# Kernel optimization log

Measured on AMD Instinct MI355X. Metric: run time of the kernel, lower is better.

The kernel has to match this reference:

```python
import jax, jax.numpy as jnp
import numpy as np

B, L, DM = 1, 512, 768
DS, DC, EX = 64, 4, 2
DI = EX * DM            # d_inner = 1536
DR = DM // 16           # dt_rank = 48


def setup_inputs() -> dict:
    key = jax.random.key(0)
    ks = jax.random.split(key, 12)
    s = 0.02
    inp = {
        "x": jax.random.normal(ks[0], (B, L, DM), dtype=jnp.float32),
        "ln_w": jnp.ones((DM,), jnp.float32),
        "ln_b": jnp.zeros((DM,), jnp.float32),
        "in_proj_w": jax.random.normal(ks[1], (2 * DI, DM), jnp.float32) * s,
        "conv_w": jax.random.normal(ks[2], (DI, 1, DC), jnp.float32) * s,
        "conv_b": jnp.zeros((DI,), jnp.float32),
        "x_proj_w": jax.random.normal(ks[3], (DR + 2 * DS, DI), jnp.float32) * s,
        "dt_proj_w": jax.random.normal(ks[4], (DI, DR), jnp.float32) * s,
        "dt_proj_b": jax.random.normal(ks[5], (DI,), jnp.float32) * s,
        "A_log": jnp.log(jnp.broadcast_to(jnp.arange(1, DS + 1, dtype=jnp.float32), (DI, DS))),
        "D": jnp.ones((DI,), jnp.float32),
        "out_proj_w": jax.random.normal(ks[6], (DM, DI), jnp.float32) * s,
    }
    return inp


def _layernorm(x, w, b, eps=1e-5):
    mu = jnp.mean(x, axis=-1, keepdims=True)
    var = jnp.mean((x - mu) ** 2, axis=-1, keepdims=True)
    return (x - mu) * jax.lax.rsqrt(var + eps) * w + b


def _causal_depthwise_conv(x, w, b):
    # x: [B, L, DI] -> conv over time, depthwise, causal (left pad DC-1)
    xc = jnp.transpose(x, (0, 2, 1))  # [B, DI, L]
    y = jax.lax.conv_general_dilated(
        xc, w, window_strides=(1,), padding=[(DC - 1, 0)],
        dimension_numbers=("NCH", "OIH", "NCH"), feature_group_count=DI)
    y = y + b[None, :, None]
    return jnp.transpose(y, (0, 2, 1))  # [B, L, DI]


def _selective_scan(deltaA, deltaB_u, C):
    # deltaA, deltaB_u: [B, L, DI, DS]; C: [B, L, DS]
    dA = jnp.transpose(deltaA, (1, 0, 2, 3))
    dBu = jnp.transpose(deltaB_u, (1, 0, 2, 3))
    Ct = jnp.transpose(C, (1, 0, 2))
    s0 = jnp.zeros(deltaA.shape[:1] + deltaA.shape[2:], deltaA.dtype).transpose(0, 1, 2)
    s0 = jnp.zeros((deltaA.shape[0], deltaA.shape[2], deltaA.shape[3]), deltaA.dtype)

    def step(s, inp):
        dA_t, dBu_t, C_t = inp
        s = dA_t * s + dBu_t                      # [B, DI, DS]
        y = jnp.einsum("bdn,bn->bd", s, C_t)      # [B, DI]
        return s, y

    _, ys = jax.lax.scan(step, s0, (dA, dBu, Ct))
    return jnp.transpose(ys, (1, 0, 2))           # [B, L, DI]


def reference(x, ln_w, ln_b, in_proj_w, conv_w, conv_b, x_proj_w,
              dt_proj_w, dt_proj_b, A_log, D, out_proj_w):
    residual = x
    h = _layernorm(x, ln_w, ln_b)
    xz = jnp.einsum("bld,ed->ble", h, in_proj_w)  # [B, L, 2*DI]
    x_in, z = jnp.split(xz, 2, axis=-1)
    x_in = jax.nn.silu(_causal_depthwise_conv(x_in, conv_w, conv_b))
    x_dbl = jnp.einsum("bld,ed->ble", x_in, x_proj_w)  # [B, L, DR+2*DS]
    dt, Bm, Cm = jnp.split(x_dbl, [DR, DR + DS], axis=-1)
    dt = jax.nn.softplus(jnp.einsum("blr,dr->bld", dt, dt_proj_w) + dt_proj_b)  # [B,L,DI]
    A = -jnp.exp(A_log)                                 # [DI, DS]
    deltaA = jnp.exp(dt[..., None] * A)                 # [B, L, DI, DS]
    deltaB_u = dt[..., None] * Bm[:, :, None, :] * x_in[..., None]
    y = _selective_scan(deltaA, deltaB_u, Cm)           # [B, L, DI]
    y = y + x_in * D
    y = y * jax.nn.silu(z)
    out = jnp.einsum("bld,ed->ble", y, out_proj_w)      # [B, L, DM]
    return residual + out
```

## Files before the change

kernel.cpp:

```cpp
#include <hip/hip_runtime.h>
#include <hip/hip_bf16.h>
#include <math.h>

#define L_SEQ 512
#define DM 768
#define DI 1536
#define DS 64
#define DC 4
#define DR 48
#define NBC 128
#define NP2 (NBC + DI)
#define NCF 4
#define TCF 128
#define LOG2E 1.44269504088896f

typedef __attribute__((ext_vector_type(8))) short short8;
typedef __attribute__((ext_vector_type(4))) float float4v;

#define J_LN 512
#define J_WI (2 * DI * DM / 1024)
#define J_WBC (NBC * DI / 1024)
#define J_WO (DM * DI / 1024)
#define J_WEFF ((DI / 64) * (DI / 64))
#define PREP_GRID (J_LN + J_WI + J_WBC + J_WO + J_WEFF)

__device__ __forceinline__ float bp_add(float p, int addr) {
  return p + __int_as_float(__builtin_amdgcn_ds_bpermute(addr, __float_as_int(p)));
}
__device__ __forceinline__ float lane_read(float v, int t) {
  return __int_as_float(__builtin_amdgcn_readlane(__float_as_int(v), t));
}
__device__ __forceinline__ short f2bf(float v) {
  __hip_bfloat16 h = __float2bfloat16(v);
  return *reinterpret_cast<short*>(&h);
}
__device__ __forceinline__ short8 cvt8f(const float* p, bool valid) {
  float4 u = *(const float4*)(p);
  float4 v = *(const float4*)(p + 4);
  short8 r;
  r[0] = f2bf(u.x); r[1] = f2bf(u.y); r[2] = f2bf(u.z); r[3] = f2bf(u.w);
  r[4] = f2bf(v.x); r[5] = f2bf(v.y); r[6] = f2bf(v.z); r[7] = f2bf(v.w);
  if (!valid) r = (short8)0;
  return r;
}
__device__ __forceinline__ void cvt_blk(const float* __restrict__ s,
                                        short* __restrict__ d, int b) {
  int i = b * 1024 + threadIdx.x * 4;
  float4 v = *(const float4*)(s + i);
  short4 o; o.x = f2bf(v.x); o.y = f2bf(v.y); o.z = f2bf(v.z); o.w = f2bf(v.w);
  *(short4*)(d + i) = o;
}

__device__ __forceinline__ float4v gemm32_core(
    const short* __restrict__ A, int lda, const short* __restrict__ B, int ldb,
    int K, int bx, int by, int lane, int w, float4v* red) {
  int ks = K >> 2;
  int kbeg = w * ks;
  int fr = lane & 15, koff = (lane >> 4) * 8;
  int m0 = by * 32, n0 = bx * 32;
  const short* pA0 = A + (size_t)(m0 + fr) * lda + koff + kbeg;
  const short* pA1 = pA0 + (size_t)16 * lda;
  const short* pB0 = B + (size_t)(n0 + fr) * ldb + koff + kbeg;
  const short* pB1 = pB0 + (size_t)16 * ldb;
  float4v acc00 = (float4v){0.f,0.f,0.f,0.f}, acc01 = acc00;
  float4v acc10 = acc00, acc11 = acc00;
  short8 a0A = *(const short8*)(pA0);      short8 a1A = *(const short8*)(pA1);
  short8 b0A = *(const short8*)(pB0);      short8 b1A = *(const short8*)(pB1);
  short8 a0B = *(const short8*)(pA0 + 32); short8 a1B = *(const short8*)(pA1 + 32);
  short8 b0B = *(const short8*)(pB0 + 32); short8 b1B = *(const short8*)(pB1 + 32);
  for (int k0 = 0; k0 < ks; k0 += 64) {
    short8 ca0 = a0A, ca1 = a1A, cb0 = b0A, cb1 = b1A;
    short8 da0 = a0B, da1 = a1B, db0 = b0B, db1 = b1B;
    int nA = k0 + 64; if (nA >= ks) nA = 0;
    int nB = k0 + 96; if (nB >= ks) nB = 32;
    a0A = *(const short8*)(pA0 + nA); a1A = *(const short8*)(pA1 + nA);
    b0A = *(const short8*)(pB0 + nA); b1A = *(const short8*)(pB1 + nA);
    a0B = *(const short8*)(pA0 + nB); a1B = *(const short8*)(pA1 + nB);
    b0B = *(const short8*)(pB0 + nB); b1B = *(const short8*)(pB1 + nB);
    acc00 = __builtin_amdgcn_mfma_f32_16x16x32_bf16(ca0, cb0, acc00, 0, 0, 0);
    acc01 = __builtin_amdgcn_mfma_f32_16x16x32_bf16(ca0, cb1, acc01, 0, 0, 0);
    acc10 = __builtin_amdgcn_mfma_f32_16x16x32_bf16(ca1, cb0, acc10, 0, 0, 0);
    acc11 = __builtin_amdgcn_mfma_f32_16x16x32_bf16(ca1, cb1, acc11, 0, 0, 0);
    acc00 = __builtin_amdgcn_mfma_f32_16x16x32_bf16(da0, db0, acc00, 0, 0, 0);
    acc01 = __builtin_amdgcn_mfma_f32_16x16x32_bf16(da0, db1, acc01, 0, 0, 0);
    acc10 = __builtin_amdgcn_mfma_f32_16x16x32_bf16(da1, db0, acc10, 0, 0, 0);
    acc11 = __builtin_amdgcn_mfma_f32_16x16x32_bf16(da1, db1, acc11, 0, 0, 0);
  }
  red[(w * 4 + 0) * 64 + lane] = acc00;
  red[(w * 4 + 1) * 64 + lane] = acc01;
  red[(w * 4 + 2) * 64 + lane] = acc10;
  red[(w * 4 + 3) * 64 + lane] = acc11;
  __syncthreads();
  float4v v = red[(0 * 4 + w) * 64 + lane];
  v = v + red[(1 * 4 + w) * 64 + lane];
  v = v + red[(2 * 4 + w) * 64 + lane];
  v = v + red[(3 * 4 + w) * 64 + lane];
  return v;
}

__device__ __forceinline__ void trans_store32(float* t, float4v v,
                                              int lrow, int lcol, int tid,
                                              float* dst, size_t ldT, int m0) {
  __syncthreads();
#pragma unroll
  for (int r = 0; r < 4; ++r) t[lcol * 33 + lrow + r] = v[r];
  __syncthreads();
  int i = tid >> 3, j = (tid & 7) * 4;
  float4 o = make_float4(t[i * 33 + j], t[i * 33 + j + 1],
                         t[i * 33 + j + 2], t[i * 33 + j + 3]);
  *(float4*)&dst[(size_t)i * ldT + m0 + j] = o;
}

__global__ __launch_bounds__(256) void prep(
    const float* __restrict__ x, const float* __restrict__ lnw,
    const float* __restrict__ lnb, short* __restrict__ h,
    const float* __restrict__ wi, short* __restrict__ wib,
    const float* __restrict__ wx, const float* __restrict__ wdt,
    short* __restrict__ wcomb, const float* __restrict__ wo,
    short* __restrict__ wob) {
  __shared__ float ls[4], ls2[4];
  int b = blockIdx.x;
  int tid = threadIdx.x, lane = tid & 63, w = tid >> 6;
  if (b < J_LN) {
    int l = b;
    const float* xr = x + l * DM;
    float s = 0.f, s2 = 0.f;
    for (int i = tid; i < DM; i += 256) { float t = xr[i]; s += t; s2 += t * t; }
#pragma unroll
    for (int off = 32; off; off >>= 1) { s += __shfl_xor(s, off); s2 += __shfl_xor(s2, off); }
    if (lane == 0) { ls[w] = s; ls2[w] = s2; }
    __syncthreads();
    s = ls[0] + ls[1] + ls[2] + ls[3];
    s2 = ls2[0] + ls2[1] + ls2[2] + ls2[3];
    float mean = s * (1.f / DM);
    float var = s2 * (1.f / DM) - mean * mean;
    float rstd = rsqrtf(var + 1e-5f);
    for (int i = tid; i < DM; i += 256)
      h[l * DM + i] = f2bf((xr[i] - mean) * rstd * lnw[i] + lnb[i]);
    return;
  }
  b -= J_LN;
  if (b < J_WI) { cvt_blk(wi, wib, b); return; }
  b -= J_WI;
  if (b < J_WBC) { cvt_blk(wx + DR * DI, wcomb, b); return; }
  b -= J_WBC;
  if (b < J_WO) { cvt_blk(wo, wob, b); return; }
  b -= J_WO;
  {
    int tm = b / (DI / 64), tn = b % (DI / 64);
    int qi = w & 1, qj = w >> 1;
    int m0 = tm * 64 + qi * 32, n0 = tn * 64 + qj * 32;
    int fr = lane & 15, koff = (lane >> 4) * 8;
    const float* pA0 = wdt + (size_t)(m0 + fr) * DR;
    const float* pA1 = pA0 + (size_t)16 * DR;
    float4v a00 = (float4v){0.f,0.f,0.f,0.f}, a01 = a00, a10 = a00, a11 = a00;
#pragma unroll
    for (int k0 = 0; k0 < 64; k0 += 32) {
      bool valid = (k0 + koff) < DR;
      int off = valid ? k0 + koff : 0;
      short8 fa0 = cvt8f(pA0 + off, valid);
      short8 fa1 = cvt8f(pA1 + off, valid);
      short8 fb0, fb1;
#pragma unroll
      for (int j = 0; j < 8; ++j) {
        int r = k0 + koff + j;
        fb0[j] = valid ? f2bf(wx[(size_t)r * DI + n0 + fr]) : (short)0;
        fb1[j] = valid ? f2bf(wx[(size_t)r * DI + n0 + 16 + fr]) : (short)0;
      }
      a00 = __builtin_amdgcn_mfma_f32_16x16x32_bf16(fa0, fb0, a00, 0, 0, 0);
      a01 = __builtin_amdgcn_mfma_f32_16x16x32_bf16(fa0, fb1, a01, 0, 0, 0);
      a10 = __builtin_amdgcn_mfma_f32_16x16x32_bf16(fa1, fb0, a10, 0, 0, 0);
      a11 = __builtin_amdgcn_mfma_f32_16x16x32_bf16(fa1, fb1, a11, 0, 0, 0);
    }
    int rb = (lane >> 4) * 4, cb = lane & 15;
#pragma unroll
    for (int r = 0; r < 4; ++r) {
      wcomb[(size_t)(NBC + m0 + rb + r) * DI + n0 + cb]      = f2bf(a00[r]);
      wcomb[(size_t)(NBC + m0 + rb + r) * DI + n0 + 16 + cb] = f2bf(a01[r]);
      wcomb[(size_t)(NBC + m0 + 16 + rb + r) * DI + n0 + cb]      = f2bf(a10[r]);
      wcomb[(size_t)(NBC + m0 + 16 + rb + r) * DI + n0 + 16 + cb] = f2bf(a11[r]);
    }
  }
}

__global__ __launch_bounds__(256) void k_inproj(const short* __restrict__ h,
                                                const short* __restrict__ wi,
                                                float* __restrict__ xz_in,
                                                float* __restrict__ zt) {
  __shared__ float4v red[16 * 64];
  int tid = threadIdx.x, lane = tid & 63, w = tid >> 6;
  float4v v = gemm32_core(h, DM, wi, DM, DM, blockIdx.x, blockIdx.y, lane, w, red);
  int lrow = ((w & 1) << 4) + ((lane >> 4) << 2);
  int lcol = ((w >> 1) << 4) + (lane & 15);
  int m0 = blockIdx.y * 32, n0 = blockIdx.x * 32;
  if (n0 < DI) {
#pragma unroll
    for (int r = 0; r < 4; ++r)
      xz_in[(size_t)(m0 + lrow + r) * DI + n0 + lcol] = v[r];
  } else {
    trans_store32((float*)red, v, lrow, lcol, tid,
                  zt + (size_t)(n0 - DI) * L_SEQ, L_SEQ, m0);
  }
}

__global__ __launch_bounds__(256) void conv_silu_kernel(const float* __restrict__ xz_in,
                                                        const float* __restrict__ cw,
                                                        const float* __restrict__ cb,
                                                        short* __restrict__ xc_bf,
                                                        float* __restrict__ xct) {
  __shared__ float t2[64 * 34];
  int tid = threadIdx.x;
  int dloc = tid & 63, lseg = tid >> 6;
  int d0 = blockIdx.x * 64, l0 = blockIdx.y * 32;
  int d = d0 + dloc;
  int lb = l0 + lseg * 8;
  float xin[11];
#pragma unroll
  for (int i = 0; i < 11; ++i) {
    int l = lb - 3 + i;
    xin[i] = (l >= 0) ? xz_in[(size_t)l * DI + d] : 0.f;
  }
  float w0 = cw[d * 4 + 0], w1 = cw[d * 4 + 1];
  float w2 = cw[d * 4 + 2], w3 = cw[d * 4 + 3];
  float bias = cb[d];
#pragma unroll
  for (int j = 0; j < 8; ++j) {
    float acc = bias;
    acc = fmaf(w0, xin[j], acc);
    acc = fmaf(w1, xin[j + 1], acc);
    acc = fmaf(w2, xin[j + 2], acc);
    acc = fmaf(w3, xin[j + 3], acc);
    float sig = 1.f / (1.f + __expf(-acc));
    float v = acc * sig;
    xc_bf[(size_t)(lb + j) * DI + d] = f2bf(v);
    t2[dloc * 34 + lseg * 8 + j] = v;
  }
  __syncthreads();
  int row = tid >> 2, j4 = (tid & 3) * 8;
  const float* src = &t2[row * 34 + j4];
  float2 o0 = *(const float2*)(src + 0);
  float2 o1 = *(const float2*)(src + 2);
  float2 o2 = *(const float2*)(src + 4);
  float2 o3 = *(const float2*)(src + 6);
  float* dst = &xct[(size_t)(d0 + row) * L_SEQ + l0 + j4];
  *(float2*)(dst + 0) = o0; *(float2*)(dst + 2) = o1;
  *(float2*)(dst + 4) = o2; *(float2*)(dst + 6) = o3;
}

__global__ __launch_bounds__(256) void k_proj2(const short* __restrict__ xc,
                                               const short* __restrict__ wcomb,
                                               float* __restrict__ xdblBC,
                                               float* __restrict__ dtt,
                                               const float* __restrict__ bias) {
  __shared__ float4v red[16 * 64];
  int tid = threadIdx.x, lane = tid & 63, w = tid >> 6;
  float4v v = gemm32_core(xc, DI, wcomb, DI, DI, blockIdx.x, blockIdx.y,
                          lane, w, red);
  int lrow = ((w & 1) << 4) + ((lane >> 4) << 2);
  int lcol = ((w >> 1) << 4) + (lane & 15);
  int m0 = blockIdx.y * 32, n0 = blockIdx.x * 32;
  if (n0 < NBC) {
    int idx = n0 + lcol;
    int pos = (idx < DS) ? (idx << 1) : (((idx - DS) << 1) | 1);
#pragma unroll
    for (int r = 0; r < 4; ++r)
      xdblBC[(size_t)(m0 + lrow + r) * NBC + pos] = v[r];
  } else {
    float bi = bias[n0 - NBC + lcol];
#pragma unroll
    for (int r = 0; r < 4; ++r) {
      float t = v[r] + bi;
      v[r] = (t > 20.f) ? t : log1pf(__expf(t));
    }
    trans_store32((float*)red, v, lrow, lcol, tid,
                  dtt + (size_t)(n0 - NBC) * L_SEQ, L_SEQ, m0);
  }
}

__global__ __launch_bounds__(512) void scan_fused(const float* __restrict__ dtt,
                                                  const float* __restrict__ xct,
                                                  const float* __restrict__ xdblBC,
                                                  const float* __restrict__ A_log,
                                                  const float* __restrict__ Dv,
                                                  const float* __restrict__ zt,
                                                  short* __restrict__ y) {
  __shared__ float Pb[8][16][67];
  __shared__ float sendL[2][4][64];
  __shared__ float dtsL[2][4];
  __shared__ float ys[2][512];
  int tid = threadIdx.x;
  int lane = tid & 63;
  int wv = tid >> 6;
  int dloc = wv >> 2;
  int c = wv & 3;
  int d = blockIdx.x * 2 + dloc;
  float A2 = -__expf(A_log[(size_t)d * DS + lane]) * LOG2E;
  int l0 = c * TCF;
  const float* dtp = dtt + (size_t)d * L_SEQ + l0;
  const float* xp  = xct + (size_t)d * L_SEQ + l0;
  const float* zp  = zt  + (size_t)d * L_SEQ + l0;
  float dtv0 = dtp[lane], dtv1 = dtp[64 + lane];
  float xv0  = xp[lane],  xv1  = xp[64 + lane];
  float zv0  = zp[lane],  zv1  = zp[64 + lane];
  float dtxv0 = dtv0 * xv0, dtxv1 = dtv1 * xv1;
  const float* pB = xdblBC + (size_t)l0 * NBC + 2 * lane;

  if (c < 3) {
    float s = 0.f;
#pragma unroll 8
    for (int t = 0; t < 64; ++t) {
      float dt_c  = lane_read(dtv0, t);
      float dtx_c = lane_read(dtxv0, t);
      float B_c   = pB[(size_t)t * NBC];
      s = fmaf(exp2f(dt_c * A2), s, dtx_c * B_c);
    }
#pragma unroll 8
    for (int t = 0; t < 64; ++t) {
      float dt_c  = lane_read(dtv1, t);
      float dtx_c = lane_read(dtxv1, t);
      float B_c   = pB[(size_t)(64 + t) * NBC];
      s = fmaf(exp2f(dt_c * A2), s, dtx_c * B_c);
    }
    float dsum = dtv0 + dtv1;
    dsum = bp_add(dsum, (lane ^ 1) << 2);  dsum = bp_add(dsum, (lane ^ 2) << 2);
    dsum = bp_add(dsum, (lane ^ 4) << 2);  dsum = bp_add(dsum, (lane ^ 8) << 2);
    dsum = bp_add(dsum, (lane ^ 16) << 2); dsum = bp_add(dsum, (lane ^ 32) << 2);
    sendL[dloc][c][lane] = s;
    if (lane == 0) dtsL[dloc][c] = dsum;
  }
  __syncthreads();

  float s = 0.f;
  for (int cc = 0; cc < c; ++cc) {
    float P = exp2f(A2 * dtsL[dloc][cc]);
    s = fmaf(P, s, sendL[dloc][cc][lane]);
  }

  float yout0 = 0.f, yout1 = 0.f;
#pragma unroll
  for (int half = 0; half < 2; ++half) {
    float dtvh  = half ? dtv1 : dtv0;
    float dtxvh = half ? dtxv1 : dtxv0;
    float yv = 0.f;
#pragma unroll
    for (int sb = 0; sb < 4; ++sb) {
      float P[16];
#pragma unroll
      for (int j = 0; j < 16; ++j) {
        int t = sb * 16 + j;
        float dt_c  = lane_read(dtvh, t);
        float dtx_c = lane_read(dtxvh, t);
        float2 bc = *(const float2*)&pB[(size_t)(half * 64 + t) * NBC];
        s = fmaf(exp2f(dt_c * A2), s, dtx_c * bc.x);
        P[j] = s * bc.y;
      }
#pragma unroll
      for (int j = 0; j < 16; ++j) Pb[wv][j][lane] = P[j];
      int t4 = lane >> 2, q = lane & 3;
      const float* row = &Pb[wv][t4][q * 16];
      float part = 0.f;
#pragma unroll
      for (int k = 0; k < 16; ++k) part += row[k];
      part = bp_add(part, (lane ^ 1) << 2);
      part = bp_add(part, (lane ^ 2) << 2);
      float got = __int_as_float(
          __builtin_amdgcn_ds_bpermute((lane & 15) << 4, __float_as_int(part)));
      yv = ((lane >> 4) == sb) ? got : yv;
    }
    if (half == 0) yout0 = yv; else yout1 = yv;
  }

  float Dd = Dv[d];
  float sig0 = 1.f / (1.f + exp2f(-zv0 * LOG2E));
  float sig1 = 1.f / (1.f + exp2f(-zv1 * LOG2E));
  ys[dloc][l0 + lane]      = (yout0 + xv0 * Dd) * (zv0 * sig0);
  ys[dloc][l0 + 64 + lane] = (yout1 + xv1 * Dd) * (zv1 * sig1);
  __syncthreads();
  int d0 = blockIdx.x * 2;
  short2 o;
  o.x = f2bf(ys[0][tid]);
  o.y = f2bf(ys[1][tid]);
  *(short2*)&y[(size_t)tid * DI + d0] = o;
}

__global__ __launch_bounds__(256) void k_outproj(const short* __restrict__ y,
                                                 const short* __restrict__ wo,
                                                 const float* __restrict__ x,
                                                 float* __restrict__ out) {
  __shared__ float4v red[16 * 64];
  int tid = threadIdx.x, lane = tid & 63, w = tid >> 6;
  float4v v = gemm32_core(y, DI, wo, DI, DI, blockIdx.x, blockIdx.y, lane, w, red);
  int lrow = ((w & 1) << 4) + ((lane >> 4) << 2);
  int lcol = ((w >> 1) << 4) + (lane & 15);
  int row = blockIdx.y * 32 + lrow, col = blockIdx.x * 32 + lcol;
#pragma unroll
  for (int r = 0; r < 4; ++r)
    out[(size_t)(row + r) * DM + col] = v[r] + x[(size_t)(row + r) * DM + col];
}

extern "C" void kernel_launch(void* const* d_in, const int* in_sizes, int n_in,
                              void* d_out, int out_size, void* d_ws, size_t ws_size,
                              hipStream_t stream) {
  const float* x         = (const float*)d_in[0];
  const float* ln_w      = (const float*)d_in[1];
  const float* ln_b      = (const float*)d_in[2];
  const float* in_proj_w = (const float*)d_in[3];
  const float* conv_w    = (const float*)d_in[4];
  const float* conv_b    = (const float*)d_in[5];
  const float* x_proj_w  = (const float*)d_in[6];
  const float* dt_proj_w = (const float*)d_in[7];
  const float* dt_proj_b = (const float*)d_in[8];
  const float* A_log     = (const float*)d_in[9];
  const float* Dv        = (const float*)d_in[10];
  const float* out_proj_w= (const float*)d_in[11];
  float* out = (float*)d_out;

  float* ws = (float*)d_ws;
  float* xz_in  = ws;
  float* zt     = xz_in + 786432;
  float* xct    = zt + 786432;
  float* dtt    = xct + 786432;
  float* xdblBC = dtt + 786432;
  float* fend   = xdblBC + 65536;
  short* h_bf   = (short*)fend;
  short* wi_bf  = h_bf + 393216;
  short* wo_bf  = wi_bf + 2359296;
  short* wcomb  = wo_bf + 1179648;
  short* xc_bf  = wcomb + 2555904;
  short* y_bf   = xc_bf + 786432;

  prep<<<PREP_GRID, 256, 0, stream>>>(x, ln_w, ln_b, h_bf, in_proj_w, wi_bf,
                                      x_proj_w, dt_proj_w, wcomb,
                                      out_proj_w, wo_bf);

  k_inproj<<<dim3(2 * DI / 32, L_SEQ / 32), 256, 0, stream>>>(h_bf, wi_bf,
                                                              xz_in, zt);

  conv_silu_kernel<<<dim3(DI / 64, L_SEQ / 32), 256, 0, stream>>>(
      xz_in, conv_w, conv_b, xc_bf, xct);

  k_proj2<<<dim3(NP2 / 32, L_SEQ / 32), 256, 0, stream>>>(
      xc_bf, wcomb, xdblBC, dtt, dt_proj_b);

  scan_fused<<<DI / 2, 512, 0, stream>>>(dtt, xct, xdblBC, A_log, Dv, zt, y_bf);

  k_outproj<<<dim3(DM / 32, L_SEQ / 32), 256, 0, stream>>>(y_bf, wo_bf, x, out);
}
```

Before: 198.0 us.

## Split scan into eight 64-step chunks with one channel per block

The selective scan now assigns one d_inner channel per block and splits the sequence into 8 chunks of 64 steps instead of 2 channels × 4 chunks of 128. Each chunk runs a shorter serial recurrence, which cuts per-wave latency on the critical path and doubles the grid size, at the cost of a longer carry-prefix step for later chunks and more redundant pre-pass work. The 2-byte bf16 output stores are now scattered, one per channel, instead of paired short2 writes staged through shared memory. exp2f with a LOG2E-prescaled A is replaced by __expf, and the LDS row reduction reads float2 pairs.

```diff
diff --git a/kernel.cpp b/kernel.cpp
--- a/kernel.cpp
+++ b/kernel.cpp
@@ -10,9 +10,8 @@
 #define DR 48
 #define NBC 128
 #define NP2 (NBC + DI)
-#define NCF 4
-#define TCF 128
-#define LOG2E 1.44269504088896f
+#define NCF 8
+#define TCF 64
 
 typedef __attribute__((ext_vector_type(8))) short short8;
 typedef __attribute__((ext_vector_type(4))) float float4v;
@@ -284,103 +283,78 @@
                                                   const float* __restrict__ Dv,
                                                   const float* __restrict__ zt,
                                                   short* __restrict__ y) {
-  __shared__ float Pb[8][16][67];
-  __shared__ float sendL[2][4][64];
-  __shared__ float dtsL[2][4];
-  __shared__ float ys[2][512];
+  __shared__ float Pb[8][16][66];
+  __shared__ float sendL[8][64];
+  __shared__ float dtsL[8];
   int tid = threadIdx.x;
   int lane = tid & 63;
-  int wv = tid >> 6;
-  int dloc = wv >> 2;
-  int c = wv & 3;
-  int d = blockIdx.x * 2 + dloc;
-  float A2 = -__expf(A_log[(size_t)d * DS + lane]) * LOG2E;
+  int c = tid >> 6;
+  int d = blockIdx.x;
+  float A = -__expf(A_log[(size_t)d * DS + lane]);
   int l0 = c * TCF;
-  const float* dtp = dtt + (size_t)d * L_SEQ + l0;
-  const float* xp  = xct + (size_t)d * L_SEQ + l0;
-  const float* zp  = zt  + (size_t)d * L_SEQ + l0;
-  float dtv0 = dtp[lane], dtv1 = dtp[64 + lane];
-  float xv0  = xp[lane],  xv1  = xp[64 + lane];
-  float zv0  = zp[lane],  zv1  = zp[64 + lane];
-  float dtxv0 = dtv0 * xv0, dtxv1 = dtv1 * xv1;
+  float dtv = dtt[(size_t)d * L_SEQ + l0 + lane];
+  float xv  = xct[(size_t)d * L_SEQ + l0 + lane];
+  float zv  = zt[(size_t)d * L_SEQ + l0 + lane];
+  float dtxv = dtv * xv;
   const float* pB = xdblBC + (size_t)l0 * NBC + 2 * lane;
 
-  if (c < 3) {
+  if (c < 7) {
     float s = 0.f;
 #pragma unroll 8
-    for (int t = 0; t < 64; ++t) {
-      float dt_c  = lane_read(dtv0, t);
-      float dtx_c = lane_read(dtxv0, t);
-      float B_c   = pB[(size_t)t * NBC];
-      s = fmaf(exp2f(dt_c * A2), s, dtx_c * B_c);
-    }
-#pragma unroll 8
-    for (int t = 0; t < 64; ++t) {
-      float dt_c  = lane_read(dtv1, t);
-      float dtx_c = lane_read(dtxv1, t);
-      float B_c   = pB[(size_t)(64 + t) * NBC];
-      s = fmaf(exp2f(dt_c * A2), s, dtx_c * B_c);
-    }
-    float dsum = dtv0 + dtv1;
+    for (int t = 0; t < TCF; ++t) {
+      float dt_c  = lane_read(dtv, t);
+      float dtx_c = lane_read(dtxv, t);
+      float2 bc = *(const float2*)&pB[(size_t)t * NBC];
+      s = fmaf(__expf(dt_c * A), s, dtx_c * bc.x);
+    }
+    float dsum = dtv;
     dsum = bp_add(dsum, (lane ^ 1) << 2);  dsum = bp_add(dsum, (lane ^ 2) << 2);
     dsum = bp_add(dsum, (lane ^ 4) << 2);  dsum = bp_add(dsum, (lane ^ 8) << 2);
     dsum = bp_add(dsum, (lane ^ 16) << 2); dsum = bp_add(dsum, (lane ^ 32) << 2);
-    sendL[dloc][c][lane] = s;
-    if (lane == 0) dtsL[dloc][c] = dsum;
+    sendL[c][lane] = s;
+    if (lane == 0) dtsL[c] = dsum;
   }
   __syncthreads();
 
   float s = 0.f;
   for (int cc = 0; cc < c; ++cc) {
-    float P = exp2f(A2 * dtsL[dloc][cc]);
-    s = fmaf(P, s, sendL[dloc][cc][lane]);
-  }
-
-  float yout0 = 0.f, yout1 = 0.f;
-#pragma unroll
-  for (int half = 0; half < 2; ++half) {
-    float dtvh  = half ? dtv1 : dtv0;
-    float dtxvh = half ? dtxv1 : dtxv0;
-    float yv = 0.f;
-#pragma unroll
-    for (int sb = 0; sb < 4; ++sb) {
-      float P[16];
-#pragma unroll
-      for (int j = 0; j < 16; ++j) {
-        int t = sb * 16 + j;
-        float dt_c  = lane_read(dtvh, t);
-        float dtx_c = lane_read(dtxvh, t);
-        float2 bc = *(const float2*)&pB[(size_t)(half * 64 + t) * NBC];
-        s = fmaf(exp2f(dt_c * A2), s, dtx_c * bc.x);
-        P[j] = s * bc.y;
-      }
-#pragma unroll
-      for (int j = 0; j < 16; ++j) Pb[wv][j][lane] = P[j];
-      int t4 = lane >> 2, q = lane & 3;
-      const float* row = &Pb[wv][t4][q * 16];
-      float part = 0.f;
-#pragma unroll
-      for (int k = 0; k < 16; ++k) part += row[k];
-      part = bp_add(part, (lane ^ 1) << 2);
-      part = bp_add(part, (lane ^ 2) << 2);
-      float got = __int_as_float(
-          __builtin_amdgcn_ds_bpermute((lane & 15) << 4, __float_as_int(part)));
-      yv = ((lane >> 4) == sb) ? got : yv;
-    }
-    if (half == 0) yout0 = yv; else yout1 = yv;
+    float P = __expf(A * dtsL[cc]);
+    s = fmaf(P, s, sendL[cc][lane]);
+  }
+
+  float yv = 0.f;
+#pragma unroll
+  for (int sb = 0; sb < 4; ++sb) {
+    float P[16];
+#pragma unroll
+    for (int j = 0; j < 16; ++j) {
+      int t = sb * 16 + j;
+      float dt_c  = lane_read(dtv, t);
+      float dtx_c = lane_read(dtxv, t);
+      float2 bc = *(const float2*)&pB[(size_t)t * NBC];
+      s = fmaf(__expf(dt_c * A), s, dtx_c * bc.x);
+      P[j] = s * bc.y;
+    }
+#pragma unroll
+    for (int j = 0; j < 16; ++j) Pb[c][j][lane] = P[j];
+    int t4 = lane >> 2, q = lane & 3;
+    const float* row = &Pb[c][t4][q * 16];
+    float part = 0.f;
+#pragma unroll
+    for (int k = 0; k < 8; ++k) {
+      float2 v2 = *(const float2*)(row + 2 * k);
+      part += v2.x + v2.y;
+    }
+    part = bp_add(part, (lane ^ 1) << 2);
+    part = bp_add(part, (lane ^ 2) << 2);
+    float got = __int_as_float(
+        __builtin_amdgcn_ds_bpermute((lane & 15) << 4, __float_as_int(part)));
+    yv = ((lane >> 4) == sb) ? got : yv;
   }
 
   float Dd = Dv[d];
-  float sig0 = 1.f / (1.f + exp2f(-zv0 * LOG2E));
-  float sig1 = 1.f / (1.f + exp2f(-zv1 * LOG2E));
-  ys[dloc][l0 + lane]      = (yout0 + xv0 * Dd) * (zv0 * sig0);
-  ys[dloc][l0 + 64 + lane] = (yout1 + xv1 * Dd) * (zv1 * sig1);
-  __syncthreads();
-  int d0 = blockIdx.x * 2;
-  short2 o;
-  o.x = f2bf(ys[0][tid]);
-  o.y = f2bf(ys[1][tid]);
-  *(short2*)&y[(size_t)tid * DI + d0] = o;
+  float sig = 1.f / (1.f + __expf(-zv));
+  y[(size_t)tid * DI + d] = f2bf((yv + xv * Dd) * (zv * sig));
 }
 
 __global__ __launch_bounds__(256) void k_outproj(const short* __restrict__ y,
@@ -442,7 +416,7 @@
   k_proj2<<<dim3(NP2 / 32, L_SEQ / 32), 256, 0, stream>>>(
       xc_bf, wcomb, xdblBC, dtt, dt_proj_b);
 
-  scan_fused<<<DI / 2, 512, 0, stream>>>(dtt, xct, xdblBC, A_log, Dv, zt, y_bf);
+  scan_fused<<<DI, 512, 0, stream>>>(dtt, xct, xdblBC, A_log, Dv, zt, y_bf);
 
   k_outproj<<<dim3(DM / 32, L_SEQ / 32), 256, 0, stream>>>(y_bf, wo_bf, x, out);
 }
```

Result: no change. 201.1 us (+1.6%).
